# Optimization experiments

Measured on AMD Instinct MI355X. Metric: run time of the kernel, lower is better.

Reference implementation:

```python
import jax, jax.numpy as jnp
import numpy as np

B, N, D, H = 8, 128, 768, 64
NEG = -1e30
SLOPE = 0.01  # LeakyReLU slope
EPS = 1e-5    # BatchNorm eps


def setup_inputs() -> dict:
    key = jax.random.key(0)
    ks = jax.random.split(key, 10)
    s = 0.02
    feature = jax.random.normal(ks[0], (B, N, D), jnp.float32)
    aspect = jax.random.normal(ks[1], (B, D), jnp.float32)
    adj = jax.random.randint(ks[2], (B, N, N), 0, 2).astype(jnp.int32)
    W0 = jax.random.normal(ks[3], (D, D), jnp.float32) * s
    b0 = jnp.zeros((D,), jnp.float32)
    W1 = jax.random.normal(ks[4], (D, D), jnp.float32) * s
    b1 = jnp.zeros((D,), jnp.float32)
    A1 = jax.random.normal(ks[5], (2 * D, H), jnp.float32) * s  # afcs[0]
    ab1 = jnp.zeros((H,), jnp.float32)
    A2 = jax.random.normal(ks[6], (H, 1), jnp.float32) * s      # afcs[2]
    ab2 = jnp.zeros((1,), jnp.float32)
    gamma = jnp.ones((D,), jnp.float32)
    beta = jnp.zeros((D,), jnp.float32)
    return dict(feature=feature, aspect=aspect, adj=adj, W0=W0, b0=b0,
                W1=W1, b1=b1, A1=A1, ab1=ab1, A2=A2, ab2=ab2,
                gamma=gamma, beta=beta)


def reference(feature, aspect, adj, W0, b0, W1, b1, A1, ab1, A2, ab2, gamma, beta):
    # aspect is unused by the original forward.
    m = adj.astype(feature.dtype)          # [B,N,N] 0/1 mask
    d = A1.shape[0] // 2
    A1s, A1t = A1[:d], A1[d:]              # weight-split of Linear(2*mem_dim, H):
                                           # [h_i, h_j] @ A1 == h_i @ A1s + h_j @ A1t
    for (W, b) in ((W0, b0), (W1, b1)):
        h = feature @ W + b                # [B,N,D]
        s_src = h @ A1s                    # [B,N,H], broadcast over j
        s_tgt = h @ A1t                    # [B,N,H], broadcast over i
        hid = jax.nn.relu(s_src[:, :, None, :] + s_tgt[:, None, :, :] + ab1)  # [B,N,N,H]
        e = (hid @ A2)[..., 0] + ab2[0]    # [B,N,N]
        e = jnp.where(e > 0, e, SLOPE * e)  # LeakyReLU(0.01)
        logits = e * m + (1.0 - m) * NEG    # mask_logits
        b_, n_ = logits.shape[0], logits.shape[1]
        # NOTE: original softmaxes over the FLATTENED N*N axis, not per-row.
        attn = jax.nn.softmax(logits.reshape(b_, n_ * n_), axis=-1).reshape(b_, n_, n_)
        feature = jnp.einsum('bij,bjd->bid', attn, h)  # attention.bmm(h)
        # dropout is identity in eval / deterministic reference
    node_feature = feature
    g = node_feature.sum(axis=1)           # [B,D]
    mean = g.mean(axis=0)
    var = g.var(axis=0)                    # biased, matches BN training forward
    graph_feature = gamma * (g - mean) / jnp.sqrt(var + EPS) + beta
    return graph_feature, node_feature
```

## Files before the change

kernel.cpp:

```cpp
#include <hip/hip_runtime.h>
#include <math.h>

#define NEG_V (-1e30f)
#define SLOPE_V 0.01f
#define EPS_V 1e-5f

typedef __attribute__((ext_vector_type(8))) short bs8;
typedef __attribute__((ext_vector_type(4))) float f32x4;

__device__ __forceinline__ void split2(float x, unsigned short& hi, unsigned short& lo) {
    unsigned u = __float_as_uint(x);
    unsigned h = (u + 0x7FFFu + ((u >> 16) & 1u)) >> 16;
    hi = (unsigned short)h;
    float hf = __uint_as_float(h << 16);
    float l = x - hf;
    unsigned ul = __float_as_uint(l);
    lo = (unsigned short)((ul + 0x7FFFu + ((ul >> 16) & 1u)) >> 16);
}

__device__ __forceinline__ void mfma_loop(
    const unsigned short* __restrict__ Ahg, const unsigned short* __restrict__ Alg,
    int lda,
    const unsigned short* __restrict__ Bhg, const unsigned short* __restrict__ Blg,
    int ldb, int K, int row0, int col0,
    f32x4 (&acc)[2][2],
    unsigned short (*buf)[64][40])
{
    const int tid = threadIdx.x;
    const int lane = tid & 63, wid = tid >> 6;
    const int wm0 = (wid >> 1) * 32, wn0 = (wid & 1) * 32;
    const int lm = lane & 15, q = lane >> 4;
    const int sr = tid >> 2, sc = (tid & 3) * 8;

    const unsigned short* pAh = Ahg + (size_t)(row0 + sr) * lda + sc;
    const unsigned short* pAl = Alg + (size_t)(row0 + sr) * lda + sc;
    const unsigned short* pBh = Bhg + (size_t)(col0 + sr) * ldb + sc;
    const unsigned short* pBl = Blg + (size_t)(col0 + sr) * ldb + sc;

    bs8 rAh = *(const bs8*)(pAh);
    bs8 rAl = *(const bs8*)(pAl);
    bs8 rBh = *(const bs8*)(pBh);
    bs8 rBl = *(const bs8*)(pBl);

    int st = 0;
    for (int k0 = 0; k0 < K; k0 += 32) {
        unsigned short (*Ah)[40] = buf[st * 4 + 0];
        unsigned short (*Al)[40] = buf[st * 4 + 1];
        unsigned short (*Bh)[40] = buf[st * 4 + 2];
        unsigned short (*Bl)[40] = buf[st * 4 + 3];
        *(bs8*)&Ah[sr][sc] = rAh;
        *(bs8*)&Al[sr][sc] = rAl;
        *(bs8*)&Bh[sr][sc] = rBh;
        *(bs8*)&Bl[sr][sc] = rBl;
        __syncthreads();
        if (k0 + 32 < K) {
            rAh = *(const bs8*)(pAh + k0 + 32);
            rAl = *(const bs8*)(pAl + k0 + 32);
            rBh = *(const bs8*)(pBh + k0 + 32);
            rBl = *(const bs8*)(pBl + k0 + 32);
        }
        bs8 a_h[2], a_l[2], b_h[2], b_l[2];
#pragma unroll
        for (int t = 0; t < 2; t++) {
            a_h[t] = *(bs8*)&Ah[wm0 + t * 16 + lm][q * 8];
            a_l[t] = *(bs8*)&Al[wm0 + t * 16 + lm][q * 8];
            b_h[t] = *(bs8*)&Bh[wn0 + t * 16 + lm][q * 8];
            b_l[t] = *(bs8*)&Bl[wn0 + t * 16 + lm][q * 8];
        }
#pragma unroll
        for (int mt = 0; mt < 2; mt++)
#pragma unroll
            for (int nt = 0; nt < 2; nt++) {
                acc[mt][nt] = __builtin_amdgcn_mfma_f32_16x16x32_bf16(a_h[mt], b_h[nt], acc[mt][nt], 0, 0, 0);
                acc[mt][nt] = __builtin_amdgcn_mfma_f32_16x16x32_bf16(a_h[mt], b_l[nt], acc[mt][nt], 0, 0, 0);
                acc[mt][nt] = __builtin_amdgcn_mfma_f32_16x16x32_bf16(a_l[mt], b_h[nt], acc[mt][nt], 0, 0, 0);
            }
        st ^= 1;
    }
}

__device__ __forceinline__ void transpose_split_tile(
    const float* __restrict__ src, int src_ld,
    unsigned short* __restrict__ dh, unsigned short* __restrict__ dl, int dst_ld,
    unsigned short (*Th)[72], unsigned short (*Tl)[72])
{
    int tid = threadIdx.x;
    int r = tid >> 2;
    int cb = (tid & 3) * 16;
#pragma unroll
    for (int cc = 0; cc < 16; cc += 4) {
        float4 v = *(const float4*)(src + (size_t)r * src_ld + cb + cc);
        unsigned short hh, ll;
        split2(v.x, hh, ll); Th[cb + cc + 0][r] = hh; Tl[cb + cc + 0][r] = ll;
        split2(v.y, hh, ll); Th[cb + cc + 1][r] = hh; Tl[cb + cc + 1][r] = ll;
        split2(v.z, hh, ll); Th[cb + cc + 2][r] = hh; Tl[cb + cc + 2][r] = ll;
        split2(v.w, hh, ll); Th[cb + cc + 3][r] = hh; Tl[cb + cc + 3][r] = ll;
    }
    __syncthreads();
    int n = tid >> 2, ch = (tid & 3) * 8;
    *(bs8*)(dh + (size_t)n * dst_ld + ch)      = *(bs8*)&Th[n][ch];
    *(bs8*)(dh + (size_t)n * dst_ld + ch + 32) = *(bs8*)&Th[n][ch + 32];
    *(bs8*)(dl + (size_t)n * dst_ld + ch)      = *(bs8*)&Tl[n][ch];
    *(bs8*)(dl + (size_t)n * dst_ld + ch + 32) = *(bs8*)&Tl[n][ch + 32];
}

__device__ __forceinline__ void flat_split_job(
    const float* __restrict__ src, unsigned short* __restrict__ dh,
    unsigned short* __restrict__ dl, size_t base)
{
    unsigned short hh, ll;
#pragma unroll
    for (int g = 0; g < 2; g++) {
        bs8 sh, sl;
#pragma unroll
        for (int cc = 0; cc < 8; cc += 4) {
            float4 v = *(const float4*)(src + base + g * 8 + cc);
            split2(v.x, hh, ll); sh[cc + 0] = (short)hh; sl[cc + 0] = (short)ll;
            split2(v.y, hh, ll); sh[cc + 1] = (short)hh; sl[cc + 1] = (short)ll;
            split2(v.z, hh, ll); sh[cc + 2] = (short)hh; sl[cc + 2] = (short)ll;
            split2(v.w, hh, ll); sh[cc + 3] = (short)hh; sl[cc + 3] = (short)ll;
        }
        *(bs8*)(dh + base + g * 8) = sh;
        *(bs8*)(dl + base + g * 8) = sl;
    }
}

__global__ __launch_bounds__(256) void prep_k(
    const float* __restrict__ W0, const float* __restrict__ W1,
    const float* __restrict__ A1, const float* __restrict__ feature,
    const float* __restrict__ b0, const float* __restrict__ b1,
    unsigned short* Wt0h, unsigned short* Wt0l,
    unsigned short* Wt1h, unsigned short* Wt1l,
    unsigned short* fh, unsigned short* fl,
    unsigned short* WAth, unsigned short* WAtl,
    float* bA)
{
    __shared__ __align__(16) char smem[20480];
    int id = blockIdx.x, tid = threadIdx.x;
    if (id < 288) {
        unsigned short (*Th)[72] = (unsigned short(*)[72])(smem);
        unsigned short (*Tl)[72] = (unsigned short(*)[72])(smem + 9216);
        if (id < 144) {
            int kt = id / 12, nt = id % 12;
            transpose_split_tile(W0 + (size_t)(kt * 64) * 768 + nt * 64, 768,
                                 Wt0h + (size_t)(nt * 64) * 768 + kt * 64,
                                 Wt0l + (size_t)(nt * 64) * 768 + kt * 64, 768, Th, Tl);
        } else {
            int r = id - 144, kt = r / 12, nt = r % 12;
            transpose_split_tile(W1 + (size_t)(kt * 64) * 768 + nt * 64, 768,
                                 Wt1h + (size_t)(nt * 64) * 768 + kt * 64,
                                 Wt1l + (size_t)(nt * 64) * 768 + kt * 64, 768, Th, Tl);
        }
    } else if (id < 480) {
        flat_split_job(feature, fh, fl, (size_t)(id - 288) * 4096 + tid * 16);
    } else if (id < 528) {
        int j = id - 480;
        int rt = j % 12, ct = (j / 12) & 1, layer = j / 24;
        const float* W = layer ? W1 : W0;
        const int r0 = rt * 64;
        unsigned short (*Ah)[40] = (unsigned short(*)[40])(smem);
        unsigned short (*Al)[40] = (unsigned short(*)[40])(smem + 5120);
        unsigned short (*Bh)[40] = (unsigned short(*)[40])(smem + 10240);
        unsigned short (*Bl)[40] = (unsigned short(*)[40])(smem + 15360);
        const int lane = tid & 63, wid = tid >> 6;
        const int wm0 = (wid >> 1) * 32, wn0 = (wid & 1) * 32;
        const int lm = lane & 15, q = lane >> 4;
        const int akk = tid & 31, acs = (tid >> 5) * 8;
        const int br = tid >> 2, bks = (tid & 3) * 8;
        f32x4 acc[2][2] = {};
        for (int k0 = 0; k0 < 768; k0 += 32) {
            {
                const float* ap = A1 + (size_t)(ct * 768 + k0 + akk) * 64 + acs;
                float4 v0 = *(const float4*)ap;
                float4 v1 = *(const float4*)(ap + 4);
                unsigned short hv, lv;
                split2(v0.x, hv, lv); Ah[acs + 0][akk] = hv; Al[acs + 0][akk] = lv;
                split2(v0.y, hv, lv); Ah[acs + 1][akk] = hv; Al[acs + 1][akk] = lv;
                split2(v0.z, hv, lv); Ah[acs + 2][akk] = hv; Al[acs + 2][akk] = lv;
                split2(v0.w, hv, lv); Ah[acs + 3][akk] = hv; Al[acs + 3][akk] = lv;
                split2(v1.x, hv, lv); Ah[acs + 4][akk] = hv; Al[acs + 4][akk] = lv;
                split2(v1.y, hv, lv); Ah[acs + 5][akk] = hv; Al[acs + 5][akk] = lv;
                split2(v1.z, hv, lv); Ah[acs + 6][akk] = hv; Al[acs + 6][akk] = lv;
                split2(v1.w, hv, lv); Ah[acs + 7][akk] = hv; Al[acs + 7][akk] = lv;
            }
            {
                const float* wp = W + (size_t)(r0 + br) * 768 + k0 + bks;
                float4 v0 = *(const float4*)wp;
                float4 v1 = *(const float4*)(wp + 4);
                bs8 sh, sl; unsigned short hv, lv;
                split2(v0.x, hv, lv); sh[0] = (short)hv; sl[0] = (short)lv;
                split2(v0.y, hv, lv); sh[1] = (short)hv; sl[1] = (short)lv;
                split2(v0.z, hv, lv); sh[2] = (short)hv; sl[2] = (short)lv;
                split2(v0.w, hv, lv); sh[3] = (short)hv; sl[3] = (short)lv;
                split2(v1.x, hv, lv); sh[4] = (short)hv; sl[4] = (short)lv;
                split2(v1.y, hv, lv); sh[5] = (short)hv; sl[5] = (short)lv;
                split2(v1.z, hv, lv); sh[6] = (short)hv; sl[6] = (short)lv;
                split2(v1.w, hv, lv); sh[7] = (short)hv; sl[7] = (short)lv;
                *(bs8*)&Bh[br][bks] = sh;
                *(bs8*)&Bl[br][bks] = sl;
            }
            __syncthreads();
            bs8 a_h[2], a_l[2], b_h[2], b_l[2];
#pragma unroll
            for (int t = 0; t < 2; t++) {
                a_h[t] = *(bs8*)&Ah[wm0 + t * 16 + lm][q * 8];
                a_l[t] = *(bs8*)&Al[wm0 + t * 16 + lm][q * 8];
                b_h[t] = *(bs8*)&Bh[wn0 + t * 16 + lm][q * 8];
                b_l[t] = *(bs8*)&Bl[wn0 + t * 16 + lm][q * 8];
            }
#pragma unroll
            for (int mt = 0; mt < 2; mt++)
#pragma unroll
                for (int nt = 0; nt < 2; nt++) {
                    acc[mt][nt] = __builtin_amdgcn_mfma_f32_16x16x32_bf16(a_h[mt], b_h[nt], acc[mt][nt], 0, 0, 0);
                    acc[mt][nt] = __builtin_amdgcn_mfma_f32_16x16x32_bf16(a_h[mt], b_l[nt], acc[mt][nt], 0, 0, 0);
                    acc[mt][nt] = __builtin_amdgcn_mfma_f32_16x16x32_bf16(a_l[mt], b_h[nt], acc[mt][nt], 0, 0, 0);
                }
            __syncthreads();
        }
        const int c0 = ct * 64;
        size_t base = (size_t)layer * 98304;
#pragma unroll
        for (int mt = 0; mt < 2; mt++)
#pragma unroll
            for (int nt = 0; nt < 2; nt++) {
                int n = r0 + wn0 + nt * 16 + lm;
#pragma unroll
                for (int i = 0; i < 4; i++) {
                    int m = c0 + wm0 + mt * 16 + q * 4 + i;
                    unsigned short hv, lv;
                    split2(acc[mt][nt][i], hv, lv);
                    WAth[base + (size_t)m * 768 + n] = hv;
                    WAtl[base + (size_t)m * 768 + n] = lv;
                }
            }
    } else {
        float* redb = (float*)(smem);
        int layer = id - 528;
        const float* bv = layer ? b1 : b0;
        int c = tid & 127, half = tid >> 7;
        float acc = 0.f;
        for (int kk = 0; kk < 384; kk++) {
            int k = half * 384 + kk;
            int row = (c < 64 ? k : 768 + k);
            acc += bv[k] * A1[(size_t)row * 64 + (c & 63)];
        }
        redb[tid] = acc;
        __syncthreads();
        if (tid < 128) bA[layer * 128 + tid] = redb[tid] + redb[tid + 128];
    }
}

__global__ __launch_bounds__(256) void gemm_fused_k(
    const unsigned short* __restrict__ Ahg, const unsigned short* __restrict__ Alg,
    const unsigned short* __restrict__ Wth, const unsigned short* __restrict__ Wtl,
    const unsigned short* __restrict__ WAth, const unsigned short* __restrict__ WAtl,
    const float* __restrict__ bias,
    unsigned short* __restrict__ hth, unsigned short* __restrict__ htl,
    float* __restrict__ s)
{
    __shared__ unsigned short smem[8][64][40];
    int bx = blockIdx.x, row0 = blockIdx.y * 64;
    const unsigned short* Bh;
    const unsigned short* Bl;
    int col0;
    if (bx < 12) { Bh = Wth;  Bl = Wtl;  col0 = bx * 64; }
    else         { Bh = WAth; Bl = WAtl; col0 = (bx - 12) * 64; }
    f32x4 acc[2][2] = {};
    mfma_loop(Ahg, Alg, 768, Bh, Bl, 768, 768, row0, col0, acc, smem);
    int tid = threadIdx.x, lane = tid & 63, wid = tid >> 6;
    int wm0 = (wid >> 1) * 32, wn0 = (wid & 1) * 32;
    int lm = lane & 15, q = lane >> 4;
    if (bx >= 12) {
#pragma unroll
        for (int mt = 0; mt < 2; mt++)
#pragma unroll
            for (int nt = 0; nt < 2; nt++) {
                int c = col0 + wn0 + nt * 16 + lm;
#pragma unroll
                for (int i = 0; i < 4; i++) {
                    int r = row0 + wm0 + mt * 16 + q * 4 + i;
                    s[(size_t)r * 128 + c] = acc[mt][nt][i];
                }
            }
        return;
    }
    __syncthreads();
    unsigned short* flat = &smem[0][0][0];
    unsigned short (*Hi)[69] = (unsigned short(*)[69])flat;
    unsigned short (*Lo)[69] = (unsigned short(*)[69])(flat + 4416);
#pragma unroll
    for (int mt = 0; mt < 2; mt++)
#pragma unroll
        for (int nt = 0; nt < 2; nt++) {
            int c = wn0 + nt * 16 + lm;
            float bv = bias[col0 + c];
#pragma unroll
            for (int i = 0; i < 4; i++) {
                int r = wm0 + mt * 16 + q * 4 + i;
                unsigned short hv, lv;
                split2(acc[mt][nt][i] + bv, hv, lv);
                Hi[r][c] = hv; Lo[r][c] = lv;
            }
        }
    __syncthreads();
    int d = tid >> 2, kq = (tid & 3) * 16;
    int b = row0 >> 7, kb = row0 & 127;
    bs8 th0, th1, tl0, tl1;
#pragma unroll
    for (int e = 0; e < 8; e++) {
        th0[e] = Hi[kq + e][d];     th1[e] = Hi[kq + 8 + e][d];
        tl0[e] = Lo[kq + e][d];     tl1[e] = Lo[kq + 8 + e][d];
    }
    size_t to = ((size_t)b * 768 + col0 + d) * 128 + kb + kq;
    *(bs8*)(hth + to) = th0; *(bs8*)(hth + to + 8) = th1;
    *(bs8*)(htl + to) = tl0; *(bs8*)(htl + to + 8) = tl1;
}

__global__ __launch_bounds__(256) void score_k(
    const float* __restrict__ s, const int* __restrict__ adj,
    const float* __restrict__ ab1, const float* __restrict__ A2,
    const float* __restrict__ ab2, const float* __restrict__ bA,
    unsigned short* __restrict__ ph, unsigned short* __restrict__ pl,
    float* __restrict__ psum)
{
    __shared__ float st[128][65];
    __shared__ float ss[4][65];
    __shared__ float a2s[64];
    __shared__ float warr[4];
    const int bx = blockIdx.x, b = blockIdx.y, tid = threadIdx.x;
    const int i0 = bx * 4;
    for (int idx = tid; idx < 8192; idx += 256) {
        int j = idx >> 6, h2 = idx & 63;
        st[j][h2] = s[(size_t)(b * 128 + j) * 128 + 64 + h2] + bA[64 + h2];
    }
    {
        int i = tid >> 6, h2 = tid & 63;
        ss[i][h2] = s[(size_t)(b * 128 + i0 + i) * 128 + h2] + bA[h2] + ab1[h2];
    }
    if (tid < 64) a2s[tid] = A2[tid];
    __syncthreads();
    const float ab2v = ab2[0];
    const int rr = tid >> 7;
    const int j = tid & 127;
    const int r0 = rr * 2, r1 = rr * 2 + 1;
    float acc0 = 0.f, acc1 = 0.f;
#pragma unroll 4
    for (int h2 = 0; h2 < 64; h2++) {
        float bb = st[j][h2];
        float cv = a2s[h2];
        acc0 = fmaf(fmaxf(ss[r0][h2] + bb, 0.f), cv, acc0);
        acc1 = fmaf(fmaxf(ss[r1][h2] + bb, 0.f), cv, acc1);
    }
    float e0 = acc0 + ab2v; e0 = (e0 > 0.f) ? e0 : SLOPE_V * e0;
    float e1 = acc1 + ab2v; e1 = (e1 > 0.f) ? e1 : SLOPE_V * e1;
    size_t o0 = (size_t)b * 16384 + (size_t)(i0 + r0) * 128 + j;
    size_t o1 = (size_t)b * 16384 + (size_t)(i0 + r1) * 128 + j;
    float v0 = adj[o0] ? expf(e0) : 0.f;
    float v1 = adj[o1] ? expf(e1) : 0.f;
    unsigned short hv, lv;
    split2(v0, hv, lv); ph[o0] = hv; pl[o0] = lv;
    split2(v1, hv, lv); ph[o1] = hv; pl[o1] = lv;
    float vs = v0 + v1;
#pragma unroll
    for (int o = 32; o > 0; o >>= 1) vs += __shfl_down(vs, o);
    if ((tid & 63) == 0) warr[tid >> 6] = vs;
    __syncthreads();
    if (tid == 0) psum[b * 32 + bx] = warr[0] + warr[1] + warr[2] + warr[3];
}

__global__ __launch_bounds__(256) void attn_mfma_k(
    const unsigned short* __restrict__ ph, const unsigned short* __restrict__ pl,
    const unsigned short* __restrict__ hth, const unsigned short* __restrict__ htl,
    const float* __restrict__ psum, float* __restrict__ node,
    unsigned short* __restrict__ nodeh, unsigned short* __restrict__ nodel)
{
    __shared__ unsigned short smem[8][64][40];
    __shared__ float sred[33];
    int b = blockIdx.z;
    int row0 = blockIdx.y * 64, col0 = blockIdx.x * 64;
    int tid = threadIdx.x;
    if (tid < 32) sred[tid] = psum[b * 32 + tid];
    __syncthreads();
    if (tid == 0) {
        float t = 0.f;
#pragma unroll
        for (int i = 0; i < 32; i++) t += sred[i];
        sred[32] = 1.0f / t;
    }
    __syncthreads();
    float alpha = sred[32];
    f32x4 acc[2][2] = {};
    mfma_loop(ph + (size_t)b * 16384, pl + (size_t)b * 16384, 128,
              hth + (size_t)b * 98304, htl + (size_t)b * 98304, 128, 128,
              row0, col0, acc, smem);
    __syncthreads();
    float* C = node + (size_t)b * 98304;
    unsigned short* flat = &smem[0][0][0];
    unsigned short (*Hi)[69] = (unsigned short(*)[69])flat;
    unsigned short (*Lo)[69] = (unsigned short(*)[69])(flat + 4416);
    int lane = tid & 63, wid = tid >> 6;
    int wm0 = (wid >> 1) * 32, wn0 = (wid & 1) * 32;
    int lm = lane & 15, q = lane >> 4;
#pragma unroll
    for (int mt = 0; mt < 2; mt++)
#pragma unroll
        for (int nt = 0; nt < 2; nt++) {
            int c = wn0 + nt * 16 + lm;
#pragma unroll
            for (int i = 0; i < 4; i++) {
                int r = wm0 + mt * 16 + q * 4 + i;
                float v = acc[mt][nt][i] * alpha;
                C[(size_t)(row0 + r) * 768 + col0 + c] = v;
                unsigned short hv, lv;
                split2(v, hv, lv);
                Hi[r][c] = hv; Lo[r][c] = lv;
            }
        }
    __syncthreads();
    int r = tid >> 2, cq = (tid & 3) * 16;
    bs8 vh0, vh1, vl0, vl1;
#pragma unroll
    for (int e = 0; e < 8; e++) {
        vh0[e] = Hi[r][cq + e];     vh1[e] = Hi[r][cq + 8 + e];
        vl0[e] = Lo[r][cq + e];     vl1[e] = Lo[r][cq + 8 + e];
    }
    size_t ro = (size_t)(b * 128 + row0 + r) * 768 + col0 + cq;
    *(bs8*)(nodeh + ro) = vh0; *(bs8*)(nodeh + ro + 8) = vh1;
    *(bs8*)(nodel + ro) = vl0; *(bs8*)(nodel + ro + 8) = vl1;
}

__global__ __launch_bounds__(512) void gsum_bnorm_k(
    const float* __restrict__ node, const float* __restrict__ gamma,
    const float* __restrict__ beta, float* __restrict__ out)
{
    __shared__ float gbuf[8][64];
    __shared__ float mean_s[64], inv_s[64];
    int tid = threadIdx.x;
    int bg = tid >> 6, dl = tid & 63;
    int d = blockIdx.x * 64 + dl;
    float v = 0.f;
    for (int i = 0; i < 128; i++)
        v += node[(size_t)(bg * 128 + i) * 768 + d];
    gbuf[bg][dl] = v;
    __syncthreads();
    if (tid < 64) {
        float m = 0.f;
#pragma unroll
        for (int b = 0; b < 8; b++) m += gbuf[b][tid];
        m *= 0.125f;
        float var = 0.f;
#pragma unroll
        for (int b = 0; b < 8; b++) { float t = gbuf[b][tid] - m; var += t * t; }
        var *= 0.125f;
        mean_s[tid] = m;
        inv_s[tid] = 1.0f / sqrtf(var + EPS_V);
    }
    __syncthreads();
    out[bg * 768 + d] = gamma[d] * (v - mean_s[dl]) * inv_s[dl] + beta[d];
}

extern "C" void kernel_launch(void* const* d_in, const int* in_sizes, int n_in,
                              void* d_out, int out_size, void* d_ws, size_t ws_size,
                              hipStream_t stream)
{
    const float* feature = (const float*)d_in[0];
    const int*   adj     = (const int*)d_in[2];
    const float* W0      = (const float*)d_in[3];
    const float* b0      = (const float*)d_in[4];
    const float* W1      = (const float*)d_in[5];
    const float* b1      = (const float*)d_in[6];
    const float* A1      = (const float*)d_in[7];
    const float* ab1     = (const float*)d_in[8];
    const float* A2      = (const float*)d_in[9];
    const float* ab2     = (const float*)d_in[10];
    const float* gamma   = (const float*)d_in[11];
    const float* beta    = (const float*)d_in[12];

    float* ws    = (float*)d_ws;
    float* s     = ws;
    float* psum  = ws + 131072;
    float* bA    = ws + 131328;
    unsigned short* u = (unsigned short*)(ws + 131584);
    unsigned short* Wt0h = u;
    unsigned short* Wt0l = Wt0h + 589824;
    unsigned short* Wt1h = Wt0l + 589824;
    unsigned short* Wt1l = Wt1h + 589824;
    unsigned short* WAth = Wt1l + 589824;
    unsigned short* WAtl = WAth + 196608;
    unsigned short* fh   = WAtl + 196608;
    unsigned short* fl   = fh + 786432;
    unsigned short* hth  = fl + 786432;
    unsigned short* htl  = hth + 786432;
    unsigned short* ndh  = htl + 786432;
    unsigned short* ndl  = ndh + 786432;
    unsigned short* ph   = ndl + 786432;
    unsigned short* pl   = ph + 131072;

    float* out       = (float*)d_out;
    float* graph_out = out;
    float* node_out  = out + 6144;

    prep_k<<<530, 256, 0, stream>>>(W0, W1, A1, feature, b0, b1,
                                    Wt0h, Wt0l, Wt1h, Wt1l,
                                    fh, fl, WAth, WAtl, bA);

    for (int layer = 0; layer < 2; layer++) {
        const unsigned short* Wth = layer ? Wt1h : Wt0h;
        const unsigned short* Wtl = layer ? Wt1l : Wt0l;
        const float* bb = layer ? b1 : b0;
        const unsigned short* Ahg = layer ? ndh : fh;
        const unsigned short* Alg = layer ? ndl : fl;
        gemm_fused_k<<<dim3(14, 16), 256, 0, stream>>>(
            Ahg, Alg, Wth, Wtl, WAth + (size_t)layer * 98304,
            WAtl + (size_t)layer * 98304, bb, hth, htl, s);
        score_k<<<dim3(32, 8), 256, 0, stream>>>(s, adj, ab1, A2, ab2,
                                                 bA + layer * 128, ph, pl, psum);
        attn_mfma_k<<<dim3(12, 2, 8), 256, 0, stream>>>(ph, pl, hth, htl, psum,
                                                        node_out, ndh, ndl);
    }
    gsum_bnorm_k<<<12, 512, 0, stream>>>(node_out, gamma, beta, graph_out);
}
```

Baseline: 175.6 us.

## Fuse all stages into one persistent kernel with software grid barriers

Replaces the sequence of eight kernel launches (prep, per-layer gemm/score/attn, bnorm) with a single persistent 256-block kernel that separates the stages with a sense-reversing atomic grid barrier. The goal is to remove launch gaps and tail idle time between the small dependent stages. The graph-sum step is also spread over 96 blocks with a workspace reduction instead of 12 blocks. The barrier relies on all 256 blocks being co-resident, which a normal launch does not guarantee. Stages that use fewer blocks leave the rest idle at each barrier.

```diff
diff --git a/kernel.cpp b/kernel.cpp
--- a/kernel.cpp
+++ b/kernel.cpp
@@ -7,6 +7,31 @@
 
 typedef __attribute__((ext_vector_type(8))) short bs8;
 typedef __attribute__((ext_vector_type(4))) float f32x4;
+
+
+__device__ unsigned g_cnt = 0;
+__device__ unsigned g_sense = 0;
+
+__device__ __forceinline__ void gridbar(unsigned& lsense) {
+    __syncthreads();
+    if (threadIdx.x == 0) {
+        unsigned my = lsense ^ 1u;
+        __threadfence();
+        unsigned v = __hip_atomic_fetch_add(&g_cnt, 1u, __ATOMIC_ACQ_REL,
+                                            __HIP_MEMORY_SCOPE_AGENT);
+        if (v == 255u) {
+            __hip_atomic_store(&g_cnt, 0u, __ATOMIC_RELAXED, __HIP_MEMORY_SCOPE_AGENT);
+            __hip_atomic_store(&g_sense, my, __ATOMIC_RELEASE, __HIP_MEMORY_SCOPE_AGENT);
+        } else {
+            while (__hip_atomic_load(&g_sense, __ATOMIC_ACQUIRE,
+                                     __HIP_MEMORY_SCOPE_AGENT) != my)
+                __builtin_amdgcn_s_sleep(2);
+        }
+        __threadfence();
+    }
+    __syncthreads();
+    lsense ^= 1u;
+}
 
 __device__ __forceinline__ void split2(float x, unsigned short& hi, unsigned short& lo) {
     unsigned u = __float_as_uint(x);
@@ -125,43 +150,37 @@
     }
 }
 
-__global__ __launch_bounds__(256) void prep_k(
-    const float* __restrict__ W0, const float* __restrict__ W1,
-    const float* __restrict__ A1, const float* __restrict__ feature,
-    const float* __restrict__ b0, const float* __restrict__ b1,
-    unsigned short* Wt0h, unsigned short* Wt0l,
-    unsigned short* Wt1h, unsigned short* Wt1l,
-    unsigned short* fh, unsigned short* fl,
-    unsigned short* WAth, unsigned short* WAtl,
-    float* bA)
-{
-    __shared__ __align__(16) char smem[20480];
-    int id = blockIdx.x, tid = threadIdx.x;
-    if (id < 288) {
-        unsigned short (*Th)[72] = (unsigned short(*)[72])(smem);
-        unsigned short (*Tl)[72] = (unsigned short(*)[72])(smem + 9216);
-        if (id < 144) {
-            int kt = id / 12, nt = id % 12;
-            transpose_split_tile(W0 + (size_t)(kt * 64) * 768 + nt * 64, 768,
-                                 Wt0h + (size_t)(nt * 64) * 768 + kt * 64,
-                                 Wt0l + (size_t)(nt * 64) * 768 + kt * 64, 768, Th, Tl);
-        } else {
-            int r = id - 144, kt = r / 12, nt = r % 12;
-            transpose_split_tile(W1 + (size_t)(kt * 64) * 768 + nt * 64, 768,
-                                 Wt1h + (size_t)(nt * 64) * 768 + kt * 64,
-                                 Wt1l + (size_t)(nt * 64) * 768 + kt * 64, 768, Th, Tl);
-        }
-    } else if (id < 480) {
-        flat_split_job(feature, fh, fl, (size_t)(id - 288) * 4096 + tid * 16);
-    } else if (id < 528) {
-        int j = id - 480;
-        int rt = j % 12, ct = (j / 12) & 1, layer = j / 24;
-        const float* W = layer ? W1 : W0;
+struct MegaArgs {
+    const float* feature; const int* adj;
+    const float* W0; const float* b0; const float* W1; const float* b1;
+    const float* A1; const float* ab1; const float* A2; const float* ab2;
+    const float* gamma; const float* beta;
+    float* s; float* psum; float* bA; float* g_ws;
+    unsigned short* Wt0h; unsigned short* Wt0l;
+    unsigned short* Wt1h; unsigned short* Wt1l;
+    unsigned short* WAth; unsigned short* WAtl;
+    unsigned short* fh;  unsigned short* fl;
+    unsigned short* hth; unsigned short* htl;
+    unsigned short* ndh; unsigned short* ndl;
+    unsigned short* ph;  unsigned short* pl;
+    float* out_graph; float* out_node;
+};
+
+__global__ __launch_bounds__(256) void mega_k(MegaArgs A) {
+    __shared__ __align__(16) char SM[41216];
+    const int bid = blockIdx.x;
+    const int tid = threadIdx.x;
+    unsigned lsense = 0;
+
+    if (bid < 48) {
+        int j = bid;
+        int rt = j % 12, ct = (j / 12) & 1, lay = j / 24;
+        const float* W = lay ? A.W1 : A.W0;
         const int r0 = rt * 64;
-        unsigned short (*Ah)[40] = (unsigned short(*)[40])(smem);
-        unsigned short (*Al)[40] = (unsigned short(*)[40])(smem + 5120);
-        unsigned short (*Bh)[40] = (unsigned short(*)[40])(smem + 10240);
-        unsigned short (*Bl)[40] = (unsigned short(*)[40])(smem + 15360);
+        unsigned short (*Ah)[40] = (unsigned short(*)[40])(SM);
+        unsigned short (*Al)[40] = (unsigned short(*)[40])(SM + 5120);
+        unsigned short (*Bh)[40] = (unsigned short(*)[40])(SM + 10240);
+        unsigned short (*Bl)[40] = (unsigned short(*)[40])(SM + 15360);
         const int lane = tid & 63, wid = tid >> 6;
         const int wm0 = (wid >> 1) * 32, wn0 = (wid & 1) * 32;
         const int lm = lane & 15, q = lane >> 4;
@@ -170,7 +189,7 @@
         f32x4 acc[2][2] = {};
         for (int k0 = 0; k0 < 768; k0 += 32) {
             {
-                const float* ap = A1 + (size_t)(ct * 768 + k0 + akk) * 64 + acs;
+                const float* ap = A.A1 + (size_t)(ct * 768 + k0 + akk) * 64 + acs;
                 float4 v0 = *(const float4*)ap;
                 float4 v1 = *(const float4*)(ap + 4);
                 unsigned short hv, lv;
@@ -219,7 +238,7 @@
             __syncthreads();
         }
         const int c0 = ct * 64;
-        size_t base = (size_t)layer * 98304;
+        size_t base = (size_t)lay * 98304;
 #pragma unroll
         for (int mt = 0; mt < 2; mt++)
 #pragma unroll
@@ -230,294 +249,305 @@
                     int m = c0 + wm0 + mt * 16 + q * 4 + i;
                     unsigned short hv, lv;
                     split2(acc[mt][nt][i], hv, lv);
-                    WAth[base + (size_t)m * 768 + n] = hv;
-                    WAtl[base + (size_t)m * 768 + n] = lv;
+                    A.WAth[base + (size_t)m * 768 + n] = hv;
+                    A.WAtl[base + (size_t)m * 768 + n] = lv;
                 }
             }
-    } else {
-        float* redb = (float*)(smem);
-        int layer = id - 528;
-        const float* bv = layer ? b1 : b0;
+    } else if (bid < 50) {
+        float* redb = (float*)(SM);
+        int lay = bid - 48;
+        const float* bv = lay ? A.b1 : A.b0;
         int c = tid & 127, half = tid >> 7;
         float acc = 0.f;
         for (int kk = 0; kk < 384; kk++) {
             int k = half * 384 + kk;
             int row = (c < 64 ? k : 768 + k);
-            acc += bv[k] * A1[(size_t)row * 64 + (c & 63)];
+            acc += bv[k] * A.A1[(size_t)row * 64 + (c & 63)];
         }
         redb[tid] = acc;
         __syncthreads();
-        if (tid < 128) bA[layer * 128 + tid] = redb[tid] + redb[tid + 128];
-    }
-}
-
-__global__ __launch_bounds__(256) void gemm_fused_k(
-    const unsigned short* __restrict__ Ahg, const unsigned short* __restrict__ Alg,
-    const unsigned short* __restrict__ Wth, const unsigned short* __restrict__ Wtl,
-    const unsigned short* __restrict__ WAth, const unsigned short* __restrict__ WAtl,
-    const float* __restrict__ bias,
-    unsigned short* __restrict__ hth, unsigned short* __restrict__ htl,
-    float* __restrict__ s)
-{
-    __shared__ unsigned short smem[8][64][40];
-    int bx = blockIdx.x, row0 = blockIdx.y * 64;
-    const unsigned short* Bh;
-    const unsigned short* Bl;
-    int col0;
-    if (bx < 12) { Bh = Wth;  Bl = Wtl;  col0 = bx * 64; }
-    else         { Bh = WAth; Bl = WAtl; col0 = (bx - 12) * 64; }
-    f32x4 acc[2][2] = {};
-    mfma_loop(Ahg, Alg, 768, Bh, Bl, 768, 768, row0, col0, acc, smem);
-    int tid = threadIdx.x, lane = tid & 63, wid = tid >> 6;
-    int wm0 = (wid >> 1) * 32, wn0 = (wid & 1) * 32;
-    int lm = lane & 15, q = lane >> 4;
-    if (bx >= 12) {
-#pragma unroll
-        for (int mt = 0; mt < 2; mt++)
-#pragma unroll
-            for (int nt = 0; nt < 2; nt++) {
-                int c = col0 + wn0 + nt * 16 + lm;
-#pragma unroll
-                for (int i = 0; i < 4; i++) {
-                    int r = row0 + wm0 + mt * 16 + q * 4 + i;
-                    s[(size_t)r * 128 + c] = acc[mt][nt][i];
+        if (tid < 128) A.bA[lay * 128 + tid] = redb[tid] + redb[tid + 128];
+    } else {
+        for (int id = bid - 50; id < 480; id += 206) {
+            if (id < 288) {
+                __syncthreads();
+                unsigned short (*Th)[72] = (unsigned short(*)[72])(SM);
+                unsigned short (*Tl)[72] = (unsigned short(*)[72])(SM + 9216);
+                if (id < 144) {
+                    int kt = id / 12, nt = id % 12;
+                    transpose_split_tile(A.W0 + (size_t)(kt * 64) * 768 + nt * 64, 768,
+                                         A.Wt0h + (size_t)(nt * 64) * 768 + kt * 64,
+                                         A.Wt0l + (size_t)(nt * 64) * 768 + kt * 64, 768, Th, Tl);
+                } else {
+                    int r = id - 144, kt = r / 12, nt = r % 12;
+                    transpose_split_tile(A.W1 + (size_t)(kt * 64) * 768 + nt * 64, 768,
+                                         A.Wt1h + (size_t)(nt * 64) * 768 + kt * 64,
+                                         A.Wt1l + (size_t)(nt * 64) * 768 + kt * 64, 768, Th, Tl);
                 }
-            }
-        return;
-    }
-    __syncthreads();
-    unsigned short* flat = &smem[0][0][0];
-    unsigned short (*Hi)[69] = (unsigned short(*)[69])flat;
-    unsigned short (*Lo)[69] = (unsigned short(*)[69])(flat + 4416);
-#pragma unroll
-    for (int mt = 0; mt < 2; mt++)
-#pragma unroll
-        for (int nt = 0; nt < 2; nt++) {
-            int c = wn0 + nt * 16 + lm;
-            float bv = bias[col0 + c];
-#pragma unroll
-            for (int i = 0; i < 4; i++) {
-                int r = wm0 + mt * 16 + q * 4 + i;
-                unsigned short hv, lv;
-                split2(acc[mt][nt][i] + bv, hv, lv);
-                Hi[r][c] = hv; Lo[r][c] = lv;
-            }
-        }
-    __syncthreads();
-    int d = tid >> 2, kq = (tid & 3) * 16;
-    int b = row0 >> 7, kb = row0 & 127;
-    bs8 th0, th1, tl0, tl1;
-#pragma unroll
-    for (int e = 0; e < 8; e++) {
-        th0[e] = Hi[kq + e][d];     th1[e] = Hi[kq + 8 + e][d];
-        tl0[e] = Lo[kq + e][d];     tl1[e] = Lo[kq + 8 + e][d];
-    }
-    size_t to = ((size_t)b * 768 + col0 + d) * 128 + kb + kq;
-    *(bs8*)(hth + to) = th0; *(bs8*)(hth + to + 8) = th1;
-    *(bs8*)(htl + to) = tl0; *(bs8*)(htl + to + 8) = tl1;
-}
-
-__global__ __launch_bounds__(256) void score_k(
-    const float* __restrict__ s, const int* __restrict__ adj,
-    const float* __restrict__ ab1, const float* __restrict__ A2,
-    const float* __restrict__ ab2, const float* __restrict__ bA,
-    unsigned short* __restrict__ ph, unsigned short* __restrict__ pl,
-    float* __restrict__ psum)
-{
-    __shared__ float st[128][65];
-    __shared__ float ss[4][65];
-    __shared__ float a2s[64];
-    __shared__ float warr[4];
-    const int bx = blockIdx.x, b = blockIdx.y, tid = threadIdx.x;
-    const int i0 = bx * 4;
-    for (int idx = tid; idx < 8192; idx += 256) {
-        int j = idx >> 6, h2 = idx & 63;
-        st[j][h2] = s[(size_t)(b * 128 + j) * 128 + 64 + h2] + bA[64 + h2];
-    }
-    {
-        int i = tid >> 6, h2 = tid & 63;
-        ss[i][h2] = s[(size_t)(b * 128 + i0 + i) * 128 + h2] + bA[h2] + ab1[h2];
-    }
-    if (tid < 64) a2s[tid] = A2[tid];
-    __syncthreads();
-    const float ab2v = ab2[0];
-    const int rr = tid >> 7;
-    const int j = tid & 127;
-    const int r0 = rr * 2, r1 = rr * 2 + 1;
-    float acc0 = 0.f, acc1 = 0.f;
+            } else {
+                flat_split_job(A.feature, A.fh, A.fl, (size_t)(id - 288) * 4096 + tid * 16);
+            }
+        }
+    }
+    gridbar(lsense);
+
+    for (int layer = 0; layer < 2; layer++) {
+        const unsigned short* Wth = layer ? A.Wt1h : A.Wt0h;
+        const unsigned short* Wtl = layer ? A.Wt1l : A.Wt0l;
+        const float* bb = layer ? A.b1 : A.b0;
+        const unsigned short* Ahg = layer ? A.ndh : A.fh;
+        const unsigned short* Alg = layer ? A.ndl : A.fl;
+        const unsigned short* WAthL = A.WAth + (size_t)layer * 98304;
+        const unsigned short* WAtlL = A.WAtl + (size_t)layer * 98304;
+        const float* bAl = A.bA + layer * 128;
+
+        if (bid < 224) {
+            unsigned short (*buf)[64][40] = (unsigned short(*)[64][40])SM;
+            int bx = bid % 14, row0 = (bid / 14) * 64;
+            const unsigned short* Bh;
+            const unsigned short* Bl;
+            int col0;
+            if (bx < 12) { Bh = Wth;   Bl = Wtl;   col0 = bx * 64; }
+            else         { Bh = WAthL; Bl = WAtlL; col0 = (bx - 12) * 64; }
+            f32x4 acc[2][2] = {};
+            mfma_loop(Ahg, Alg, 768, Bh, Bl, 768, 768, row0, col0, acc, buf);
+            int lane = tid & 63, wid = tid >> 6;
+            int wm0 = (wid >> 1) * 32, wn0 = (wid & 1) * 32;
+            int lm = lane & 15, q = lane >> 4;
+            if (bx >= 12) {
+#pragma unroll
+                for (int mt = 0; mt < 2; mt++)
+#pragma unroll
+                    for (int nt = 0; nt < 2; nt++) {
+                        int c = col0 + wn0 + nt * 16 + lm;
+#pragma unroll
+                        for (int i = 0; i < 4; i++) {
+                            int r = row0 + wm0 + mt * 16 + q * 4 + i;
+                            A.s[(size_t)r * 128 + c] = acc[mt][nt][i];
+                        }
+                    }
+            } else {
+                __syncthreads();
+                unsigned short* flat = (unsigned short*)SM;
+                unsigned short (*Hi)[69] = (unsigned short(*)[69])flat;
+                unsigned short (*Lo)[69] = (unsigned short(*)[69])(flat + 4416);
+#pragma unroll
+                for (int mt = 0; mt < 2; mt++)
+#pragma unroll
+                    for (int nt = 0; nt < 2; nt++) {
+                        int c = wn0 + nt * 16 + lm;
+                        float bv = bb[col0 + c];
+#pragma unroll
+                        for (int i = 0; i < 4; i++) {
+                            int r = wm0 + mt * 16 + q * 4 + i;
+                            unsigned short hv, lv;
+                            split2(acc[mt][nt][i] + bv, hv, lv);
+                            Hi[r][c] = hv; Lo[r][c] = lv;
+                        }
+                    }
+                __syncthreads();
+                int d = tid >> 2, kq = (tid & 3) * 16;
+                int bN = row0 >> 7, kb = row0 & 127;
+                bs8 th0, th1, tl0, tl1;
+#pragma unroll
+                for (int e = 0; e < 8; e++) {
+                    th0[e] = Hi[kq + e][d];     th1[e] = Hi[kq + 8 + e][d];
+                    tl0[e] = Lo[kq + e][d];     tl1[e] = Lo[kq + 8 + e][d];
+                }
+                size_t to = ((size_t)bN * 768 + col0 + d) * 128 + kb + kq;
+                *(bs8*)(A.hth + to) = th0; *(bs8*)(A.hth + to + 8) = th1;
+                *(bs8*)(A.htl + to) = tl0; *(bs8*)(A.htl + to + 8) = tl1;
+            }
+        }
+        gridbar(lsense);
+
+        {
+            float (*st)[65] = (float(*)[65])SM;
+            float (*ss)[65] = (float(*)[65])(SM + 33280);
+            float* a2s = (float*)(SM + 34320);
+            float* warr = (float*)(SM + 34576);
+            int bx = bid & 31, b = bid >> 5;
+            int i0 = bx * 4;
+#pragma unroll
+            for (int g = 0; g < 8; g++) {
+                int idx4 = tid + g * 256;
+                int j = idx4 >> 4;
+                int h2 = (idx4 & 15) * 4;
+                float4 v = *(const float4*)&A.s[(size_t)(b * 128 + j) * 128 + 64 + h2];
+                float4 bv = *(const float4*)&bAl[64 + h2];
+                st[j][h2 + 0] = v.x + bv.x;
+                st[j][h2 + 1] = v.y + bv.y;
+                st[j][h2 + 2] = v.z + bv.z;
+                st[j][h2 + 3] = v.w + bv.w;
+            }
+            {
+                int i = tid >> 6, h2 = tid & 63;
+                ss[i][h2] = A.s[(size_t)(b * 128 + i0 + i) * 128 + h2] + bAl[h2] + A.ab1[h2];
+            }
+            if (tid < 64) a2s[tid] = A.A2[tid];
+            __syncthreads();
+            const float ab2v = A.ab2[0];
+            const int rr = tid >> 7;
+            const int j = tid & 127;
+            const int r0 = rr * 2, r1 = rr * 2 + 1;
+            float acc0 = 0.f, acc1 = 0.f;
 #pragma unroll 4
-    for (int h2 = 0; h2 < 64; h2++) {
-        float bb = st[j][h2];
-        float cv = a2s[h2];
-        acc0 = fmaf(fmaxf(ss[r0][h2] + bb, 0.f), cv, acc0);
-        acc1 = fmaf(fmaxf(ss[r1][h2] + bb, 0.f), cv, acc1);
-    }
-    float e0 = acc0 + ab2v; e0 = (e0 > 0.f) ? e0 : SLOPE_V * e0;
-    float e1 = acc1 + ab2v; e1 = (e1 > 0.f) ? e1 : SLOPE_V * e1;
-    size_t o0 = (size_t)b * 16384 + (size_t)(i0 + r0) * 128 + j;
-    size_t o1 = (size_t)b * 16384 + (size_t)(i0 + r1) * 128 + j;
-    float v0 = adj[o0] ? expf(e0) : 0.f;
-    float v1 = adj[o1] ? expf(e1) : 0.f;
-    unsigned short hv, lv;
-    split2(v0, hv, lv); ph[o0] = hv; pl[o0] = lv;
-    split2(v1, hv, lv); ph[o1] = hv; pl[o1] = lv;
-    float vs = v0 + v1;
-#pragma unroll
-    for (int o = 32; o > 0; o >>= 1) vs += __shfl_down(vs, o);
-    if ((tid & 63) == 0) warr[tid >> 6] = vs;
-    __syncthreads();
-    if (tid == 0) psum[b * 32 + bx] = warr[0] + warr[1] + warr[2] + warr[3];
-}
-
-__global__ __launch_bounds__(256) void attn_mfma_k(
-    const unsigned short* __restrict__ ph, const unsigned short* __restrict__ pl,
-    const unsigned short* __restrict__ hth, const unsigned short* __restrict__ htl,
-    const float* __restrict__ psum, float* __restrict__ node,
-    unsigned short* __restrict__ nodeh, unsigned short* __restrict__ nodel)
-{
-    __shared__ unsigned short smem[8][64][40];
-    __shared__ float sred[33];
-    int b = blockIdx.z;
-    int row0 = blockIdx.y * 64, col0 = blockIdx.x * 64;
-    int tid = threadIdx.x;
-    if (tid < 32) sred[tid] = psum[b * 32 + tid];
-    __syncthreads();
-    if (tid == 0) {
-        float t = 0.f;
-#pragma unroll
-        for (int i = 0; i < 32; i++) t += sred[i];
-        sred[32] = 1.0f / t;
-    }
-    __syncthreads();
-    float alpha = sred[32];
-    f32x4 acc[2][2] = {};
-    mfma_loop(ph + (size_t)b * 16384, pl + (size_t)b * 16384, 128,
-              hth + (size_t)b * 98304, htl + (size_t)b * 98304, 128, 128,
-              row0, col0, acc, smem);
-    __syncthreads();
-    float* C = node + (size_t)b * 98304;
-    unsigned short* flat = &smem[0][0][0];
-    unsigned short (*Hi)[69] = (unsigned short(*)[69])flat;
-    unsigned short (*Lo)[69] = (unsigned short(*)[69])(flat + 4416);
-    int lane = tid & 63, wid = tid >> 6;
-    int wm0 = (wid >> 1) * 32, wn0 = (wid & 1) * 32;
-    int lm = lane & 15, q = lane >> 4;
-#pragma unroll
-    for (int mt = 0; mt < 2; mt++)
-#pragma unroll
-        for (int nt = 0; nt < 2; nt++) {
-            int c = wn0 + nt * 16 + lm;
-#pragma unroll
-            for (int i = 0; i < 4; i++) {
-                int r = wm0 + mt * 16 + q * 4 + i;
-                float v = acc[mt][nt][i] * alpha;
-                C[(size_t)(row0 + r) * 768 + col0 + c] = v;
-                unsigned short hv, lv;
-                split2(v, hv, lv);
-                Hi[r][c] = hv; Lo[r][c] = lv;
-            }
-        }
-    __syncthreads();
-    int r = tid >> 2, cq = (tid & 3) * 16;
-    bs8 vh0, vh1, vl0, vl1;
-#pragma unroll
-    for (int e = 0; e < 8; e++) {
-        vh0[e] = Hi[r][cq + e];     vh1[e] = Hi[r][cq + 8 + e];
-        vl0[e] = Lo[r][cq + e];     vl1[e] = Lo[r][cq + 8 + e];
-    }
-    size_t ro = (size_t)(b * 128 + row0 + r) * 768 + col0 + cq;
-    *(bs8*)(nodeh + ro) = vh0; *(bs8*)(nodeh + ro + 8) = vh1;
-    *(bs8*)(nodel + ro) = vl0; *(bs8*)(nodel + ro + 8) = vl1;
-}
-
-__global__ __launch_bounds__(512) void gsum_bnorm_k(
-    const float* __restrict__ node, const float* __restrict__ gamma,
-    const float* __restrict__ beta, float* __restrict__ out)
-{
-    __shared__ float gbuf[8][64];
-    __shared__ float mean_s[64], inv_s[64];
-    int tid = threadIdx.x;
-    int bg = tid >> 6, dl = tid & 63;
-    int d = blockIdx.x * 64 + dl;
-    float v = 0.f;
-    for (int i = 0; i < 128; i++)
-        v += node[(size_t)(bg * 128 + i) * 768 + d];
-    gbuf[bg][dl] = v;
-    __syncthreads();
-    if (tid < 64) {
-        float m = 0.f;
-#pragma unroll
-        for (int b = 0; b < 8; b++) m += gbuf[b][tid];
+            for (int h2 = 0; h2 < 64; h2++) {
+                float bbv = st[j][h2];
+                float cv = a2s[h2];
+                acc0 = fmaf(fmaxf(ss[r0][h2] + bbv, 0.f), cv, acc0);
+                acc1 = fmaf(fmaxf(ss[r1][h2] + bbv, 0.f), cv, acc1);
+            }
+            float e0 = acc0 + ab2v; e0 = (e0 > 0.f) ? e0 : SLOPE_V * e0;
+            float e1 = acc1 + ab2v; e1 = (e1 > 0.f) ? e1 : SLOPE_V * e1;
+            size_t o0 = (size_t)b * 16384 + (size_t)(i0 + r0) * 128 + j;
+            size_t o1 = (size_t)b * 16384 + (size_t)(i0 + r1) * 128 + j;
+            float v0 = A.adj[o0] ? expf(e0) : 0.f;
+            float v1 = A.adj[o1] ? expf(e1) : 0.f;
+            unsigned short hv, lv;
+            split2(v0, hv, lv); A.ph[o0] = hv; A.pl[o0] = lv;
+            split2(v1, hv, lv); A.ph[o1] = hv; A.pl[o1] = lv;
+            float vs = v0 + v1;
+#pragma unroll
+            for (int o = 32; o > 0; o >>= 1) vs += __shfl_down(vs, o);
+            if ((tid & 63) == 0) warr[tid >> 6] = vs;
+            __syncthreads();
+            if (tid == 0) A.psum[b * 32 + bx] = warr[0] + warr[1] + warr[2] + warr[3];
+        }
+        gridbar(lsense);
+
+        if (bid < 192) {
+            unsigned short (*buf)[64][40] = (unsigned short(*)[64][40])SM;
+            float* sred = (float*)(SM + 40960);
+            int cx = bid % 12, ry = (bid / 12) & 1, b = bid / 24;
+            int row0 = ry * 64, col0 = cx * 64;
+            if (tid < 32) sred[tid] = A.psum[b * 32 + tid];
+            __syncthreads();
+            if (tid == 0) {
+                float t = 0.f;
+#pragma unroll
+                for (int i = 0; i < 32; i++) t += sred[i];
+                sred[32] = 1.0f / t;
+            }
+            __syncthreads();
+            float alpha = sred[32];
+            f32x4 acc[2][2] = {};
+            mfma_loop(A.ph + (size_t)b * 16384, A.pl + (size_t)b * 16384, 128,
+                      A.hth + (size_t)b * 98304, A.htl + (size_t)b * 98304, 128, 128,
+                      row0, col0, acc, buf);
+            __syncthreads();
+            float* C = A.out_node + (size_t)b * 98304;
+            unsigned short* flat = (unsigned short*)SM;
+            unsigned short (*Hi)[69] = (unsigned short(*)[69])flat;
+            unsigned short (*Lo)[69] = (unsigned short(*)[69])(flat + 4416);
+            int lane = tid & 63, wid = tid >> 6;
+            int wm0 = (wid >> 1) * 32, wn0 = (wid & 1) * 32;
+            int lm = lane & 15, q = lane >> 4;
+#pragma unroll
+            for (int mt = 0; mt < 2; mt++)
+#pragma unroll
+                for (int nt = 0; nt < 2; nt++) {
+                    int c = wn0 + nt * 16 + lm;
+#pragma unroll
+                    for (int i = 0; i < 4; i++) {
+                        int r = wm0 + mt * 16 + q * 4 + i;
+                        float v = acc[mt][nt][i] * alpha;
+                        C[(size_t)(row0 + r) * 768 + col0 + c] = v;
+                        unsigned short hv, lv;
+                        split2(v, hv, lv);
+                        Hi[r][c] = hv; Lo[r][c] = lv;
+                    }
+                }
+            __syncthreads();
+            int r = tid >> 2, cq = (tid & 3) * 16;
+            bs8 vh0, vh1, vl0, vl1;
+#pragma unroll
+            for (int e = 0; e < 8; e++) {
+                vh0[e] = Hi[r][cq + e];     vh1[e] = Hi[r][cq + 8 + e];
+                vl0[e] = Lo[r][cq + e];     vl1[e] = Lo[r][cq + 8 + e];
+            }
+            size_t ro = (size_t)(b * 128 + row0 + r) * 768 + col0 + cq;
+            *(bs8*)(A.ndh + ro) = vh0; *(bs8*)(A.ndh + ro + 8) = vh1;
+            *(bs8*)(A.ndl + ro) = vl0; *(bs8*)(A.ndl + ro + 8) = vl1;
+        }
+        gridbar(lsense);
+    }
+
+    if (bid < 96) {
+        float (*gbuf)[64] = (float(*)[64])SM;
+        int b = bid / 12, dt = bid % 12;
+        int dl = tid & 63, rg = tid >> 6;
+        const float* np = A.out_node + (size_t)(b * 128 + rg * 32) * 768 + dt * 64 + dl;
+        float v = 0.f;
+        for (int i = 0; i < 32; i++) v += np[(size_t)i * 768];
+        gbuf[rg][dl] = v;
+        __syncthreads();
+        if (tid < 64)
+            A.g_ws[b * 768 + dt * 64 + tid] =
+                gbuf[0][tid] + gbuf[1][tid] + gbuf[2][tid] + gbuf[3][tid];
+    }
+    gridbar(lsense);
+
+    if (bid < 12 && tid < 64) {
+        int d = bid * 64 + tid;
+        float vals[8]; float m = 0.f;
+#pragma unroll
+        for (int b = 0; b < 8; b++) { vals[b] = A.g_ws[b * 768 + d]; m += vals[b]; }
         m *= 0.125f;
         float var = 0.f;
 #pragma unroll
-        for (int b = 0; b < 8; b++) { float t = gbuf[b][tid] - m; var += t * t; }
+        for (int b = 0; b < 8; b++) { float t = vals[b] - m; var += t * t; }
         var *= 0.125f;
-        mean_s[tid] = m;
-        inv_s[tid] = 1.0f / sqrtf(var + EPS_V);
-    }
-    __syncthreads();
-    out[bg * 768 + d] = gamma[d] * (v - mean_s[dl]) * inv_s[dl] + beta[d];
+        float inv = 1.0f / sqrtf(var + EPS_V);
+        float gm = A.gamma[d], bt = A.beta[d];
+#pragma unroll
+        for (int b = 0; b < 8; b++)
+            A.out_graph[b * 768 + d] = gm * (vals[b] - m) * inv + bt;
+    }
 }
 
 extern "C" void kernel_launch(void* const* d_in, const int* in_sizes, int n_in,
                               void* d_out, int out_size, void* d_ws, size_t ws_size,
                               hipStream_t stream)
 {
-    const float* feature = (const float*)d_in[0];
-    const int*   adj     = (const int*)d_in[2];
-    const float* W0      = (const float*)d_in[3];
-    const float* b0      = (const float*)d_in[4];
-    const float* W1      = (const float*)d_in[5];
-    const float* b1      = (const float*)d_in[6];
-    const float* A1      = (const float*)d_in[7];
-    const float* ab1     = (const float*)d_in[8];
-    const float* A2      = (const float*)d_in[9];
-    const float* ab2     = (const float*)d_in[10];
-    const float* gamma   = (const float*)d_in[11];
-    const float* beta    = (const float*)d_in[12];
-
-    float* ws    = (float*)d_ws;
-    float* s     = ws;
-    float* psum  = ws + 131072;
-    float* bA    = ws + 131328;
-    unsigned short* u = (unsigned short*)(ws + 131584);
-    unsigned short* Wt0h = u;
-    unsigned short* Wt0l = Wt0h + 589824;
-    unsigned short* Wt1h = Wt0l + 589824;
-    unsigned short* Wt1l = Wt1h + 589824;
-    unsigned short* WAth = Wt1l + 589824;
-    unsigned short* WAtl = WAth + 196608;
-    unsigned short* fh   = WAtl + 196608;
-    unsigned short* fl   = fh + 786432;
-    unsigned short* hth  = fl + 786432;
-    unsigned short* htl  = hth + 786432;
-    unsigned short* ndh  = htl + 786432;
-    unsigned short* ndl  = ndh + 786432;
-    unsigned short* ph   = ndl + 786432;
-    unsigned short* pl   = ph + 131072;
-
-    float* out       = (float*)d_out;
-    float* graph_out = out;
-    float* node_out  = out + 6144;
-
-    prep_k<<<530, 256, 0, stream>>>(W0, W1, A1, feature, b0, b1,
-                                    Wt0h, Wt0l, Wt1h, Wt1l,
-                                    fh, fl, WAth, WAtl, bA);
-
-    for (int layer = 0; layer < 2; layer++) {
-        const unsigned short* Wth = layer ? Wt1h : Wt0h;
-        const unsigned short* Wtl = layer ? Wt1l : Wt0l;
-        const float* bb = layer ? b1 : b0;
-        const unsigned short* Ahg = layer ? ndh : fh;
-        const unsigned short* Alg = layer ? ndl : fl;
-        gemm_fused_k<<<dim3(14, 16), 256, 0, stream>>>(
-            Ahg, Alg, Wth, Wtl, WAth + (size_t)layer * 98304,
-            WAtl + (size_t)layer * 98304, bb, hth, htl, s);
-        score_k<<<dim3(32, 8), 256, 0, stream>>>(s, adj, ab1, A2, ab2,
-                                                 bA + layer * 128, ph, pl, psum);
-        attn_mfma_k<<<dim3(12, 2, 8), 256, 0, stream>>>(ph, pl, hth, htl, psum,
-                                                        node_out, ndh, ndl);
-    }
-    gsum_bnorm_k<<<12, 512, 0, stream>>>(node_out, gamma, beta, graph_out);
-}
+    float* ws = (float*)d_ws;
+    MegaArgs M;
+    M.feature = (const float*)d_in[0];
+    M.adj     = (const int*)d_in[2];
+    M.W0      = (const float*)d_in[3];
+    M.b0      = (const float*)d_in[4];
+    M.W1      = (const float*)d_in[5];
+    M.b1      = (const float*)d_in[6];
+    M.A1      = (const float*)d_in[7];
+    M.ab1     = (const float*)d_in[8];
+    M.A2      = (const float*)d_in[9];
+    M.ab2     = (const float*)d_in[10];
+    M.gamma   = (const float*)d_in[11];
+    M.beta    = (const float*)d_in[12];
+
+    M.s    = ws;
+    M.psum = ws + 131072;
+    M.bA   = ws + 131328;
+    M.g_ws = ws + 131584;
+    unsigned short* u = (unsigned short*)(ws + 137728);
+    M.Wt0h = u;
+    M.Wt0l = M.Wt0h + 589824;
+    M.Wt1h = M.Wt0l + 589824;
+    M.Wt1l = M.Wt1h + 589824;
+    M.WAth = M.Wt1l + 589824;
+    M.WAtl = M.WAth + 196608;
+    M.fh   = M.WAtl + 196608;
+    M.fl   = M.fh + 786432;
+    M.hth  = M.fl + 786432;
+    M.htl  = M.hth + 786432;
+    M.ndh  = M.htl + 786432;
+    M.ndl  = M.ndh + 786432;
+    M.ph   = M.ndl + 786432;
+    M.pl   = M.ph + 131072;
+
+    float* out  = (float*)d_out;
+    M.out_graph = out;
+    M.out_node  = out + 6144;
+
+    mega_k<<<256, 256, 0, stream>>>(M);
+}
```

Measured after the change: 498.5 us. 2.84x slower.
